# Kernel optimization log

Hardware: AMD Instinct MI355X
Metric: run time of the kernel (lower is better)

The kernel has to match this reference:

```python
import jax, jax.numpy as jnp
import numpy as np

# Involution2D config (matches init_kwargs)
F = 256          # filters
K = 3            # kernel_size
G = 16           # groups
RR = 4           # reduce_ratio
BN_EPS = 1e-3    # keras BatchNormalization default epsilon


def setup_inputs() -> dict:
    key = jax.random.key(0)
    ks = jax.random.split(key, 8)
    C = 256
    Cr = F // RR                    # reduce_mapping channels = 64
    KKG = K * K * G                 # span_mapping channels = 144
    s = lambda k, sh, fan: jax.random.normal(k, sh, jnp.float32) * (1.0 / np.sqrt(fan))
    return {
        "x": jax.random.normal(ks[0], (4, 128, 128, C), jnp.float32),
        # reduce_mapping: 1x1 conv + BN(inference) + relu
        "Wr": s(ks[1], (C, Cr), C),
        "br": jnp.zeros((Cr,), jnp.float32),
        "gamma": jnp.ones((Cr,), jnp.float32),
        "beta": jnp.zeros((Cr,), jnp.float32),
        "mean": jax.random.normal(ks[2], (Cr,), jnp.float32) * 0.1,
        "var": jax.random.uniform(ks[3], (Cr,), jnp.float32, 0.5, 1.5),
        # span_mapping: 1x1 conv -> K*K*G dynamic weights
        "Ws": s(ks[4], (Cr, KKG), Cr),
        "bs": jnp.zeros((KKG,), jnp.float32),
        # initial_mapping: 1x1 conv -> F (applied since F != K*K*G)
        "Wi": s(ks[5], (C, F), C),
        "bi": jnp.zeros((F,), jnp.float32),
    }


def reference(x, Wr, br, gamma, beta, mean, var, Ws, bs, Wi, bi):
    B, H, W, _ = x.shape
    KK = K * K
    # reduce_mapping: 1x1 conv + BN(inference) + relu
    r = jnp.einsum('bhwc,cd->bhwd', x, Wr) + br
    r = jax.nn.relu((r - mean) * jax.lax.rsqrt(var + BN_EPS) * gamma + beta)
    # span_mapping: per-pixel dynamic kernel weights [B,H,W,KK*G] -> [B,H,W,G,1,KK]
    w = jnp.einsum('bhwd,dk->bhwk', r, Ws) + bs
    w = w.reshape(B, H, W, G, KK)[:, :, :, :, None, :]
    # initial_mapping: 1x1 conv -> F channels
    xi = jnp.einsum('bhwc,cf->bhwf', x, Wi) + bi
    # tf.image.extract_patches (SAME, stride=1, rate=1): layout is
    # (kernel_pos major, channel minor), i.e. flat index = kpos*F + c
    pad = (K - 1) // 2
    xp = jnp.pad(xi, ((0, 0), (pad, pad), (pad, pad), (0, 0)))
    patches = jnp.stack(
        [xp[:, i:i + H, j:j + W, :] for i in range(K) for j in range(K)],
        axis=3)                                   # [B,H,W,KK,F]
    # faithful to the original K.reshape of the flat [KK*F] axis
    patches = patches.reshape(B, H, W, G, F // G, KK)
    out = jnp.sum(w * patches, axis=-1)           # [B,H,W,G,F//G]
    return out.reshape(B, H, W, F)
```

## Files before the change

### kernel.cpp

```cpp
#include <hip/hip_runtime.h>

#define BN_EPS 1e-3f

typedef __attribute__((ext_vector_type(8))) short bf16x8;
typedef __attribute__((ext_vector_type(4))) float f32x4;

__device__ inline unsigned short f2b(float f) {
    unsigned int u = __float_as_uint(f);
    unsigned int r = (u + 0x7fffu + ((u >> 16) & 1u)) >> 16;
    return (unsigned short)r;
}
__device__ inline float b2f(unsigned short h) {
    return __uint_as_float(((unsigned int)h) << 16);
}

__global__ void k_prep(const float* __restrict__ Wi, const float* __restrict__ Wr,
                       const float* __restrict__ Ws,
                       unsigned short* __restrict__ Bt, unsigned short* __restrict__ Wst) {
    int t = blockIdx.x * 256 + threadIdx.x;
    if (t < 320 * 256) {
        int n = t >> 8, k = t & 255;
        float v = (n < 256) ? Wi[k * 256 + n] : Wr[k * 64 + (n - 256)];
        Bt[t] = f2b(v);
    } else {
        int t2 = t - 320 * 256;
        if (t2 < 144 * 64) {
            int n = t2 >> 6, k = t2 & 63;
            Wst[t2] = f2b(Ws[k * 144 + n]);
        }
    }
}

#define XIP 264
#define RS_OFF (180 * XIP)
#define RSP 72
#define WL_OFF (RS_OFF + 180 * RSP)
#define SMN (WL_OFF + 128 * 144)

__global__ __launch_bounds__(512, 2) void k_fused(
    const float* __restrict__ x, const unsigned short* __restrict__ Bt,
    const unsigned short* __restrict__ Wst,
    const float* __restrict__ bi, const float* __restrict__ br,
    const float* __restrict__ gamma, const float* __restrict__ beta,
    const float* __restrict__ mean, const float* __restrict__ var,
    const float* __restrict__ bs, float* __restrict__ out)
{
    __shared__ __attribute__((aligned(16))) unsigned short sm[SMN];
    const int tid = threadIdx.x;
    const int bx = blockIdx.x;
    const int w0 = (bx & 7) * 16;
    const int h0 = ((bx >> 3) & 15) * 8;
    const int bb = bx >> 7;

    const int wv = tid >> 6;
    const int lane = tid & 63;
    const int col = lane & 15;
    const int quad = lane >> 4;

    const float bi_v0 = bi[(2 * wv) * 16 + col];
    const float bi_v1 = bi[(2 * wv + 1) * 16 + col];
    const int dcl = (wv & 3) * 16 + col;
    const float brd = br[dcl];
    const float md  = mean[dcl];
    const float sc  = gamma[dcl] * rsqrtf(var[dcl] + BN_EPS);
    const float btv = beta[dcl];

    bf16x8 bx0[8], bx1[8], brr[8];
    {
        const unsigned short* p0 = &Bt[((2 * wv) * 16 + col) * 256];
        const unsigned short* p1 = &Bt[((2 * wv + 1) * 16 + col) * 256];
#pragma unroll
        for (int kc = 0; kc < 8; ++kc) {
            bx0[kc] = *(const bf16x8*)&p0[kc * 32 + quad * 8];
            bx1[kc] = *(const bf16x8*)&p1[kc * 32 + quad * 8];
        }
        if (wv < 4) {
            const unsigned short* pr = &Bt[((16 + wv) * 16 + col) * 256];
#pragma unroll
            for (int kc = 0; kc < 8; ++kc)
                brr[kc] = *(const bf16x8*)&pr[kc * 32 + quad * 8];
        }
    }

    const int chq = (tid & 15) * 4;

    float4 vcur[4];
    int hp_cur;
    {
        hp_cur = (tid >> 4);
        int r = hp_cur / 18, cc = hp_cur - r * 18;
        int gh = h0 - 1 + r, gw = w0 - 1 + cc;
        bool ok = (hp_cur < 180) && ((unsigned)gh < 128u) && ((unsigned)gw < 128u);
        if (ok) {
            const float* src = x + (((long long)(bb * 128 + gh)) * 128 + gw) * 256 + chq;
#pragma unroll
            for (int j = 0; j < 4; ++j) vcur[j] = *(const float4*)&src[j * 64];
        } else {
#pragma unroll
            for (int j = 0; j < 4; ++j) vcur[j] = (float4){0.f, 0.f, 0.f, 0.f};
        }
        if (hp_cur < 180) {
#pragma unroll
            for (int j = 0; j < 4; ++j) {
                uint2 pk;
                pk.x = (unsigned)f2b(vcur[j].x) | ((unsigned)f2b(vcur[j].y) << 16);
                pk.y = (unsigned)f2b(vcur[j].z) | ((unsigned)f2b(vcur[j].w) << 16);
                *(uint2*)&sm[hp_cur * XIP + chq + j * 64] = pk;
            }
        }
    }
    __syncthreads();

    for (int c = 0; c < 6; ++c) {
        float4 vn[4];
        int hp_n = 192;
        if (c < 5) {
            hp_n = (c + 1) * 32 + (tid >> 4);
            int r = hp_n / 18, cc = hp_n - r * 18;
            int gh = h0 - 1 + r, gw = w0 - 1 + cc;
            bool ok = (hp_n < 180) && ((unsigned)gh < 128u) && ((unsigned)gw < 128u);
            if (ok) {
                const float* src = x + (((long long)(bb * 128 + gh)) * 128 + gw) * 256 + chq;
#pragma unroll
                for (int j = 0; j < 4; ++j) vn[j] = *(const float4*)&src[j * 64];
            } else {
#pragma unroll
                for (int j = 0; j < 4; ++j) vn[j] = (float4){0.f, 0.f, 0.f, 0.f};
            }
        }

        f32x4 a00 = {0.f,0.f,0.f,0.f}, a01 = a00, a10 = a00, a11 = a00;
        f32x4 ar0 = a00, ar1 = a00;
        {
            const int rowA0 = (c * 32 + col) * XIP;
            const int rowA1 = (c * 32 + 16 + col) * XIP;
#pragma unroll
            for (int kc = 0; kc < 8; ++kc) {
                const int kb = kc * 32 + quad * 8;
                bf16x8 a0 = *(const bf16x8*)&sm[rowA0 + kb];
                bf16x8 a1 = *(const bf16x8*)&sm[rowA1 + kb];
                a00 = __builtin_amdgcn_mfma_f32_16x16x32_bf16(a0, bx0[kc], a00, 0, 0, 0);
                a10 = __builtin_amdgcn_mfma_f32_16x16x32_bf16(a1, bx0[kc], a10, 0, 0, 0);
                a01 = __builtin_amdgcn_mfma_f32_16x16x32_bf16(a0, bx1[kc], a01, 0, 0, 0);
                a11 = __builtin_amdgcn_mfma_f32_16x16x32_bf16(a1, bx1[kc], a11, 0, 0, 0);
                if (wv < 4) {
                    ar0 = __builtin_amdgcn_mfma_f32_16x16x32_bf16(a0, brr[kc], ar0, 0, 0, 0);
                    ar1 = __builtin_amdgcn_mfma_f32_16x16x32_bf16(a1, brr[kc], ar1, 0, 0, 0);
                }
            }
        }
        __syncthreads();

        if (c < 5 && hp_n < 180) {
#pragma unroll
            for (int j = 0; j < 4; ++j) {
                uint2 pk;
                pk.x = (unsigned)f2b(vn[j].x) | ((unsigned)f2b(vn[j].y) << 16);
                pk.y = (unsigned)f2b(vn[j].z) | ((unsigned)f2b(vn[j].w) << 16);
                *(uint2*)&sm[hp_n * XIP + chq + j * 64] = pk;
            }
        }

        {
            const int n0 = (2 * wv) * 16 + col;
            const int n1 = (2 * wv + 1) * 16 + col;
            const int rb = c * 32 + quad * 4;
#pragma unroll
            for (int rg = 0; rg < 4; ++rg) {
                const int r0 = rb + rg, r1 = rb + 16 + rg;
                if (r0 < 180) {
                    sm[r0 * XIP + n0] = f2b(a00[rg] + bi_v0);
                    sm[r0 * XIP + n1] = f2b(a01[rg] + bi_v1);
                }
                if (r1 < 180) {
                    sm[r1 * XIP + n0] = f2b(a10[rg] + bi_v0);
                    sm[r1 * XIP + n1] = f2b(a11[rg] + bi_v1);
                }
            }
            if (wv < 4) {
#pragma unroll
                for (int rg = 0; rg < 4; ++rg) {
                    const int r0 = rb + rg, r1 = rb + 16 + rg;
                    if (r0 < 180) {
                        float v = (ar0[rg] + brd - md) * sc + btv;
                        sm[RS_OFF + r0 * RSP + dcl] = f2b(fmaxf(v, 0.f));
                    }
                    if (r1 < 180) {
                        float v = (ar1[rg] + brd - md) * sc + btv;
                        sm[RS_OFF + r1 * RSP + dcl] = f2b(fmaxf(v, 0.f));
                    }
                }
            }
        }
        __syncthreads();
    }

    {
        f32x4 wacc[9];
#pragma unroll
        for (int j = 0; j < 9; ++j) wacc[j] = (f32x4){0.f, 0.f, 0.f, 0.f};
        const int arow = (19 + wv * 18 + col) * RSP;
#pragma unroll
        for (int kc = 0; kc < 2; ++kc) {
            const int kb = kc * 32 + quad * 8;
            bf16x8 ra = *(const bf16x8*)&sm[RS_OFF + arow + kb];
#pragma unroll
            for (int j = 0; j < 9; ++j) {
                bf16x8 wb = *(const bf16x8*)&Wst[(j * 16 + col) * 64 + kb];
                wacc[j] = __builtin_amdgcn_mfma_f32_16x16x32_bf16(ra, wb, wacc[j], 0, 0, 0);
            }
        }
#pragma unroll
        for (int j = 0; j < 9; ++j) {
            const int n = j * 16 + col;
            const float bv = bs[n];
            const int prow = wv * 16 + quad * 4;
#pragma unroll
            for (int rg = 0; rg < 4; ++rg)
                sm[WL_OFF + (prow + rg) * 144 + n] = f2b(wacc[j][rg] + bv);
        }
    }
    __syncthreads();

    {
        const int g = tid & 15;
        const int pb = tid >> 4;

        const int idx0 = g * 144;
        const int kp0  = idx0 >> 8;
        const int c0   = idx0 & 255;
        int len1 = 256 - c0; if (len1 > 144) len1 = 144;
        const int kp1  = kp0 + 1;
        const int koff0 = (kp0 / 3) * 18 + (kp0 % 3);
        const int koff1 = (kp1 <= 8) ? ((kp1 / 3) * 18 + (kp1 % 3)) : 0;

#pragma unroll
        for (int jj = 0; jj < 4; ++jj) {
            const int p = pb + 32 * jj;
            const int phb = (p >> 4) * 18 + (p & 15);
            const int base0 = (phb + koff0) * XIP + c0;
            const int base1 = (phb + koff1) * XIP;

            float wf[9];
#pragma unroll
            for (int kk = 0; kk < 9; ++kk)
                wf[kk] = b2f(sm[WL_OFF + p * 144 + g * 9 + kk]);

            float res[16];
            {
                int4 xv[9];
#pragma unroll
                for (int i = 0; i < 9; ++i) {
                    const int e = i * 8;
                    const int addr = (e < len1) ? (base0 + e) : (base1 + (e - len1));
                    xv[i] = *(const int4*)&sm[addr];
                }
#pragma unroll
                for (int f2 = 0; f2 < 8; ++f2) {
                    float a = 0.f;
#pragma unroll
                    for (int kk = 0; kk < 9; ++kk) {
                        const int e = f2 * 9 + kk;
                        const int word = ((const int*)&xv[e >> 3])[(e >> 1) & 3];
                        const unsigned short u = (e & 1) ? (unsigned short)(((unsigned)word) >> 16)
                                                         : (unsigned short)(word & 0xffff);
                        a += wf[kk] * b2f(u);
                    }
                    res[f2] = a;
                }
            }
            {
                int4 xv[9];
#pragma unroll
                for (int i = 9; i < 18; ++i) {
                    const int e = i * 8;
                    const int addr = (e < len1) ? (base0 + e) : (base1 + (e - len1));
                    xv[i - 9] = *(const int4*)&sm[addr];
                }
#pragma unroll
                for (int f2 = 8; f2 < 16; ++f2) {
                    float a = 0.f;
#pragma unroll
                    for (int kk = 0; kk < 9; ++kk) {
                        const int e = f2 * 9 + kk;
                        const int i = (e >> 3) - 9;
                        const int word = ((const int*)&xv[i])[(e >> 1) & 3];
                        const unsigned short u = (e & 1) ? (unsigned short)(((unsigned)word) >> 16)
                                                         : (unsigned short)(word & 0xffff);
                        a += wf[kk] * b2f(u);
                    }
                    res[f2] = a;
                }
            }

            const long long orow =
                (((long long)(bb * 128 + h0 + (p >> 4))) * 128 + (w0 + (p & 15))) * 256 + g * 16;
#pragma unroll
            for (int q = 0; q < 4; ++q) {
                float4 o = {res[q * 4 + 0], res[q * 4 + 1], res[q * 4 + 2], res[q * 4 + 3]};
                *(float4*)&out[orow + q * 4] = o;
            }
        }
    }
}

extern "C" void kernel_launch(void* const* d_in, const int* in_sizes, int n_in,
                              void* d_out, int out_size, void* d_ws, size_t ws_size,
                              hipStream_t stream) {
    const float* x     = (const float*)d_in[0];
    const float* Wr    = (const float*)d_in[1];
    const float* br    = (const float*)d_in[2];
    const float* gamma = (const float*)d_in[3];
    const float* beta  = (const float*)d_in[4];
    const float* mean  = (const float*)d_in[5];
    const float* var   = (const float*)d_in[6];
    const float* Ws    = (const float*)d_in[7];
    const float* bs    = (const float*)d_in[8];
    const float* Wi    = (const float*)d_in[9];
    const float* bi    = (const float*)d_in[10];
    float* out = (float*)d_out;

    unsigned char* ws = (unsigned char*)d_ws;
    unsigned short* Bt  = (unsigned short*)(ws + 0);
    unsigned short* Wst = (unsigned short*)(ws + 163840);

    k_prep<<<dim3(356), dim3(256), 0, stream>>>(Wi, Wr, Ws, Bt, Wst);
    k_fused<<<dim3(512), dim3(512), 0, stream>>>(
        x, Bt, Wst, bi, br, gamma, beta, mean, var, bs, out);
}
```

Measured before the change: 174.8 us.

## Double block to 1024 threads, giving each wave one output tile per stage

Grows the fused block from 8 to 16 waves. Each wave now computes one 16-column tile of the initial-mapping GEMM instead of two, and the x staging loads are spread across twice as many threads. The span-mapping GEMM is split between two wave halves, with one column tile computed redundantly by both. The involution stage handles half as many pixels per thread. The aim is more waves per CU to hide latency, since LDS use already limits the CU to one block. The risk is that the stricter launch bounds force fewer registers per thread and cause spills.

```diff
diff --git a/kernel.cpp b/kernel.cpp
--- a/kernel.cpp
+++ b/kernel.cpp
@@ -37,7 +37,7 @@
 #define WL_OFF (RS_OFF + 180 * RSP)
 #define SMN (WL_OFF + 128 * 144)
 
-__global__ __launch_bounds__(512, 2) void k_fused(
+__global__ __launch_bounds__(1024, 4) void k_fused(
     const float* __restrict__ x, const unsigned short* __restrict__ Bt,
     const unsigned short* __restrict__ Wst,
     const float* __restrict__ bi, const float* __restrict__ br,
@@ -57,23 +57,19 @@
     const int col = lane & 15;
     const int quad = lane >> 4;
 
-    const float bi_v0 = bi[(2 * wv) * 16 + col];
-    const float bi_v1 = bi[(2 * wv + 1) * 16 + col];
+    const float bi_v = bi[wv * 16 + col];
     const int dcl = (wv & 3) * 16 + col;
     const float brd = br[dcl];
     const float md  = mean[dcl];
     const float sc  = gamma[dcl] * rsqrtf(var[dcl] + BN_EPS);
     const float btv = beta[dcl];
 
-    bf16x8 bx0[8], bx1[8], brr[8];
+    bf16x8 bxA[8], brr[8];
     {
-        const unsigned short* p0 = &Bt[((2 * wv) * 16 + col) * 256];
-        const unsigned short* p1 = &Bt[((2 * wv + 1) * 16 + col) * 256];
-#pragma unroll
-        for (int kc = 0; kc < 8; ++kc) {
-            bx0[kc] = *(const bf16x8*)&p0[kc * 32 + quad * 8];
-            bx1[kc] = *(const bf16x8*)&p1[kc * 32 + quad * 8];
-        }
+        const unsigned short* p0 = &Bt[(wv * 16 + col) * 256];
+#pragma unroll
+        for (int kc = 0; kc < 8; ++kc)
+            bxA[kc] = *(const bf16x8*)&p0[kc * 32 + quad * 8];
         if (wv < 4) {
             const unsigned short* pr = &Bt[((16 + wv) * 16 + col) * 256];
 #pragma unroll
@@ -82,67 +78,62 @@
         }
     }
 
-    const int chq = (tid & 15) * 4;
-
-    float4 vcur[4];
-    int hp_cur;
+    const int chq = (tid & 31) * 4;
+
     {
-        hp_cur = (tid >> 4);
-        int r = hp_cur / 18, cc = hp_cur - r * 18;
+        int hp = tid >> 5;
+        int r = hp / 18, cc = hp - r * 18;
         int gh = h0 - 1 + r, gw = w0 - 1 + cc;
-        bool ok = (hp_cur < 180) && ((unsigned)gh < 128u) && ((unsigned)gw < 128u);
+        bool ok = ((unsigned)gh < 128u) && ((unsigned)gw < 128u);
+        float4 v0, v1;
         if (ok) {
             const float* src = x + (((long long)(bb * 128 + gh)) * 128 + gw) * 256 + chq;
-#pragma unroll
-            for (int j = 0; j < 4; ++j) vcur[j] = *(const float4*)&src[j * 64];
+            v0 = *(const float4*)&src[0];
+            v1 = *(const float4*)&src[128];
         } else {
-#pragma unroll
-            for (int j = 0; j < 4; ++j) vcur[j] = (float4){0.f, 0.f, 0.f, 0.f};
-        }
-        if (hp_cur < 180) {
-#pragma unroll
-            for (int j = 0; j < 4; ++j) {
-                uint2 pk;
-                pk.x = (unsigned)f2b(vcur[j].x) | ((unsigned)f2b(vcur[j].y) << 16);
-                pk.y = (unsigned)f2b(vcur[j].z) | ((unsigned)f2b(vcur[j].w) << 16);
-                *(uint2*)&sm[hp_cur * XIP + chq + j * 64] = pk;
-            }
-        }
+            v0 = (float4){0.f, 0.f, 0.f, 0.f};
+            v1 = v0;
+        }
+        uint2 pk;
+        pk.x = (unsigned)f2b(v0.x) | ((unsigned)f2b(v0.y) << 16);
+        pk.y = (unsigned)f2b(v0.z) | ((unsigned)f2b(v0.w) << 16);
+        *(uint2*)&sm[hp * XIP + chq] = pk;
+        pk.x = (unsigned)f2b(v1.x) | ((unsigned)f2b(v1.y) << 16);
+        pk.y = (unsigned)f2b(v1.z) | ((unsigned)f2b(v1.w) << 16);
+        *(uint2*)&sm[hp * XIP + chq + 128] = pk;
     }
     __syncthreads();
 
     for (int c = 0; c < 6; ++c) {
-        float4 vn[4];
+        float4 vn0, vn1;
         int hp_n = 192;
         if (c < 5) {
-            hp_n = (c + 1) * 32 + (tid >> 4);
+            hp_n = (c + 1) * 32 + (tid >> 5);
             int r = hp_n / 18, cc = hp_n - r * 18;
             int gh = h0 - 1 + r, gw = w0 - 1 + cc;
             bool ok = (hp_n < 180) && ((unsigned)gh < 128u) && ((unsigned)gw < 128u);
             if (ok) {
                 const float* src = x + (((long long)(bb * 128 + gh)) * 128 + gw) * 256 + chq;
-#pragma unroll
-                for (int j = 0; j < 4; ++j) vn[j] = *(const float4*)&src[j * 64];
+                vn0 = *(const float4*)&src[0];
+                vn1 = *(const float4*)&src[128];
             } else {
-#pragma unroll
-                for (int j = 0; j < 4; ++j) vn[j] = (float4){0.f, 0.f, 0.f, 0.f};
-            }
-        }
-
-        f32x4 a00 = {0.f,0.f,0.f,0.f}, a01 = a00, a10 = a00, a11 = a00;
-        f32x4 ar0 = a00, ar1 = a00;
+                vn0 = (float4){0.f, 0.f, 0.f, 0.f};
+                vn1 = vn0;
+            }
+        }
+
+        f32x4 acc0 = {0.f, 0.f, 0.f, 0.f}, acc1 = acc0;
+        f32x4 ar0 = acc0, ar1 = acc0;
         {
             const int rowA0 = (c * 32 + col) * XIP;
-            const int rowA1 = (c * 32 + 16 + col) * XIP;
+            const int rowA1 = rowA0 + 16 * XIP;
 #pragma unroll
             for (int kc = 0; kc < 8; ++kc) {
                 const int kb = kc * 32 + quad * 8;
                 bf16x8 a0 = *(const bf16x8*)&sm[rowA0 + kb];
                 bf16x8 a1 = *(const bf16x8*)&sm[rowA1 + kb];
-                a00 = __builtin_amdgcn_mfma_f32_16x16x32_bf16(a0, bx0[kc], a00, 0, 0, 0);
-                a10 = __builtin_amdgcn_mfma_f32_16x16x32_bf16(a1, bx0[kc], a10, 0, 0, 0);
-                a01 = __builtin_amdgcn_mfma_f32_16x16x32_bf16(a0, bx1[kc], a01, 0, 0, 0);
-                a11 = __builtin_amdgcn_mfma_f32_16x16x32_bf16(a1, bx1[kc], a11, 0, 0, 0);
+                acc0 = __builtin_amdgcn_mfma_f32_16x16x32_bf16(a0, bxA[kc], acc0, 0, 0, 0);
+                acc1 = __builtin_amdgcn_mfma_f32_16x16x32_bf16(a1, bxA[kc], acc1, 0, 0, 0);
                 if (wv < 4) {
                     ar0 = __builtin_amdgcn_mfma_f32_16x16x32_bf16(a0, brr[kc], ar0, 0, 0, 0);
                     ar1 = __builtin_amdgcn_mfma_f32_16x16x32_bf16(a1, brr[kc], ar1, 0, 0, 0);
@@ -152,35 +143,28 @@
         __syncthreads();
 
         if (c < 5 && hp_n < 180) {
-#pragma unroll
-            for (int j = 0; j < 4; ++j) {
-                uint2 pk;
-                pk.x = (unsigned)f2b(vn[j].x) | ((unsigned)f2b(vn[j].y) << 16);
-                pk.y = (unsigned)f2b(vn[j].z) | ((unsigned)f2b(vn[j].w) << 16);
-                *(uint2*)&sm[hp_n * XIP + chq + j * 64] = pk;
-            }
+            uint2 pk;
+            pk.x = (unsigned)f2b(vn0.x) | ((unsigned)f2b(vn0.y) << 16);
+            pk.y = (unsigned)f2b(vn0.z) | ((unsigned)f2b(vn0.w) << 16);
+            *(uint2*)&sm[hp_n * XIP + chq] = pk;
+            pk.x = (unsigned)f2b(vn1.x) | ((unsigned)f2b(vn1.y) << 16);
+            pk.y = (unsigned)f2b(vn1.z) | ((unsigned)f2b(vn1.w) << 16);
+            *(uint2*)&sm[hp_n * XIP + chq + 128] = pk;
         }
 
         {
-            const int n0 = (2 * wv) * 16 + col;
-            const int n1 = (2 * wv + 1) * 16 + col;
+            const int n0 = wv * 16 + col;
             const int rb = c * 32 + quad * 4;
 #pragma unroll
             for (int rg = 0; rg < 4; ++rg) {
-                const int r0 = rb + rg, r1 = rb + 16 + rg;
-                if (r0 < 180) {
-                    sm[r0 * XIP + n0] = f2b(a00[rg] + bi_v0);
-                    sm[r0 * XIP + n1] = f2b(a01[rg] + bi_v1);
-                }
-                if (r1 < 180) {
-                    sm[r1 * XIP + n0] = f2b(a10[rg] + bi_v0);
-                    sm[r1 * XIP + n1] = f2b(a11[rg] + bi_v1);
-                }
+                const int r0 = rb + rg, r1 = r0 + 16;
+                if (r0 < 180) sm[r0 * XIP + n0] = f2b(acc0[rg] + bi_v);
+                if (r1 < 180) sm[r1 * XIP + n0] = f2b(acc1[rg] + bi_v);
             }
             if (wv < 4) {
 #pragma unroll
                 for (int rg = 0; rg < 4; ++rg) {
-                    const int r0 = rb + rg, r1 = rb + 16 + rg;
+                    const int r0 = rb + rg, r1 = r0 + 16;
                     if (r0 < 180) {
                         float v = (ar0[rg] + brd - md) * sc + btv;
                         sm[RS_OFF + r0 * RSP + dcl] = f2b(fmaxf(v, 0.f));
@@ -196,28 +180,30 @@
     }
 
     {
-        f32x4 wacc[9];
-#pragma unroll
-        for (int j = 0; j < 9; ++j) wacc[j] = (f32x4){0.f, 0.f, 0.f, 0.f};
-        const int arow = (19 + wv * 18 + col) * RSP;
+        const int m = wv & 7;
+        const int jbase = (wv >> 3) * 4;
+        f32x4 wacc[5];
+#pragma unroll
+        for (int jj = 0; jj < 5; ++jj) wacc[jj] = (f32x4){0.f, 0.f, 0.f, 0.f};
+        const int arow = (19 + m * 18 + col) * RSP;
 #pragma unroll
         for (int kc = 0; kc < 2; ++kc) {
             const int kb = kc * 32 + quad * 8;
             bf16x8 ra = *(const bf16x8*)&sm[RS_OFF + arow + kb];
 #pragma unroll
-            for (int j = 0; j < 9; ++j) {
-                bf16x8 wb = *(const bf16x8*)&Wst[(j * 16 + col) * 64 + kb];
-                wacc[j] = __builtin_amdgcn_mfma_f32_16x16x32_bf16(ra, wb, wacc[j], 0, 0, 0);
-            }
-        }
-#pragma unroll
-        for (int j = 0; j < 9; ++j) {
-            const int n = j * 16 + col;
+            for (int jj = 0; jj < 5; ++jj) {
+                bf16x8 wb = *(const bf16x8*)&Wst[((jbase + jj) * 16 + col) * 64 + kb];
+                wacc[jj] = __builtin_amdgcn_mfma_f32_16x16x32_bf16(ra, wb, wacc[jj], 0, 0, 0);
+            }
+        }
+#pragma unroll
+        for (int jj = 0; jj < 5; ++jj) {
+            const int n = (jbase + jj) * 16 + col;
             const float bv = bs[n];
-            const int prow = wv * 16 + quad * 4;
+            const int prow = m * 16 + quad * 4;
 #pragma unroll
             for (int rg = 0; rg < 4; ++rg)
-                sm[WL_OFF + (prow + rg) * 144 + n] = f2b(wacc[j][rg] + bv);
+                sm[WL_OFF + (prow + rg) * 144 + n] = f2b(wacc[jj][rg] + bv);
         }
     }
     __syncthreads();
@@ -235,8 +221,8 @@
         const int koff1 = (kp1 <= 8) ? ((kp1 / 3) * 18 + (kp1 % 3)) : 0;
 
 #pragma unroll
-        for (int jj = 0; jj < 4; ++jj) {
-            const int p = pb + 32 * jj;
+        for (int jj = 0; jj < 2; ++jj) {
+            const int p = pb + 64 * jj;
             const int phb = (p >> 4) * 18 + (p & 15);
             const int base0 = (phb + koff0) * XIP + c0;
             const int base1 = (phb + koff1) * XIP;
@@ -325,6 +311,6 @@
     unsigned short* Wst = (unsigned short*)(ws + 163840);
 
     k_prep<<<dim3(356), dim3(256), 0, stream>>>(Wi, Wr, Ws, Bt, Wst);
-    k_fused<<<dim3(512), dim3(512), 0, stream>>>(
+    k_fused<<<dim3(512), dim3(1024), 0, stream>>>(
         x, Bt, Wst, bi, br, gamma, beta, mean, var, bs, out);
 }
```

Result: slower. 179.1 us (+2.4%).

## Split fused involution kernel into GEMM pass and halo gather pass

Applied to the files above, without the earlier changes.

The single fused kernel, which recomputed the 1x1 projections over a halo of 180 pixels per 128-pixel tile, is split into two kernels. The first computes xi and the dynamic weights for 64 pixels per block without halo and writes them to the workspace as bf16. The second gathers an 8x8 tile plus halo from global memory and applies the involution. This removes redundant halo GEMM work and cuts shared memory so more blocks fit per CU, at the cost of a round trip through global memory of about 50 MB of intermediates and an extra launch.

```diff
diff --git a/kernel.cpp b/kernel.cpp
--- a/kernel.cpp
+++ b/kernel.cpp
@@ -31,193 +31,177 @@
     }
 }
 
-#define XIP 264
-#define RS_OFF (180 * XIP)
-#define RSP 72
-#define WL_OFF (RS_OFF + 180 * RSP)
-#define SMN (WL_OFF + 128 * 144)
-
-__global__ __launch_bounds__(512, 2) void k_fused(
+#define AXIP 264
+#define ARS_OFF (64 * AXIP)
+#define ASMN (ARS_OFF + 64 * 72)
+
+__global__ __launch_bounds__(256, 3) void k_xiw(
     const float* __restrict__ x, const unsigned short* __restrict__ Bt,
     const unsigned short* __restrict__ Wst,
     const float* __restrict__ bi, const float* __restrict__ br,
     const float* __restrict__ gamma, const float* __restrict__ beta,
     const float* __restrict__ mean, const float* __restrict__ var,
-    const float* __restrict__ bs, float* __restrict__ out)
+    const float* __restrict__ bs,
+    unsigned short* __restrict__ xi_g, unsigned short* __restrict__ w_g)
 {
-    __shared__ __attribute__((aligned(16))) unsigned short sm[SMN];
+    __shared__ __attribute__((aligned(16))) unsigned short sm[ASMN];
     const int tid = threadIdx.x;
-    const int bx = blockIdx.x;
-    const int w0 = (bx & 7) * 16;
-    const int h0 = ((bx >> 3) & 15) * 8;
-    const int bb = bx >> 7;
+    const long long px0 = (long long)blockIdx.x * 64;
 
     const int wv = tid >> 6;
     const int lane = tid & 63;
     const int col = lane & 15;
     const int quad = lane >> 4;
 
-    const float bi_v0 = bi[(2 * wv) * 16 + col];
-    const float bi_v1 = bi[(2 * wv + 1) * 16 + col];
-    const int dcl = (wv & 3) * 16 + col;
-    const float brd = br[dcl];
-    const float md  = mean[dcl];
-    const float sc  = gamma[dcl] * rsqrtf(var[dcl] + BN_EPS);
-    const float btv = beta[dcl];
-
-    bf16x8 bx0[8], bx1[8], brr[8];
-    {
-        const unsigned short* p0 = &Bt[((2 * wv) * 16 + col) * 256];
-        const unsigned short* p1 = &Bt[((2 * wv + 1) * 16 + col) * 256];
-#pragma unroll
-        for (int kc = 0; kc < 8; ++kc) {
-            bx0[kc] = *(const bf16x8*)&p0[kc * 32 + quad * 8];
-            bx1[kc] = *(const bf16x8*)&p1[kc * 32 + quad * 8];
-        }
-        if (wv < 4) {
-            const unsigned short* pr = &Bt[((16 + wv) * 16 + col) * 256];
-#pragma unroll
-            for (int kc = 0; kc < 8; ++kc)
-                brr[kc] = *(const bf16x8*)&pr[kc * 32 + quad * 8];
-        }
-    }
-
-    const int chq = (tid & 15) * 4;
-
-    float4 vcur[4];
-    int hp_cur;
-    {
-        hp_cur = (tid >> 4);
-        int r = hp_cur / 18, cc = hp_cur - r * 18;
-        int gh = h0 - 1 + r, gw = w0 - 1 + cc;
-        bool ok = (hp_cur < 180) && ((unsigned)gh < 128u) && ((unsigned)gw < 128u);
-        if (ok) {
-            const float* src = x + (((long long)(bb * 128 + gh)) * 128 + gw) * 256 + chq;
-#pragma unroll
-            for (int j = 0; j < 4; ++j) vcur[j] = *(const float4*)&src[j * 64];
+#pragma unroll
+    for (int it = 0; it < 8; ++it) {
+        const int flat = it * 256 + tid;
+        const int px = flat >> 5;
+        const int cho = (flat & 31) * 8;
+        const float* src = x + (px0 + px) * 256 + cho;
+        float4 v0 = *(const float4*)&src[0];
+        float4 v1 = *(const float4*)&src[4];
+        int4 pk;
+        pk.x = (int)((unsigned)f2b(v0.x) | ((unsigned)f2b(v0.y) << 16));
+        pk.y = (int)((unsigned)f2b(v0.z) | ((unsigned)f2b(v0.w) << 16));
+        pk.z = (int)((unsigned)f2b(v1.x) | ((unsigned)f2b(v1.y) << 16));
+        pk.w = (int)((unsigned)f2b(v1.z) | ((unsigned)f2b(v1.w) << 16));
+        *(int4*)&sm[px * AXIP + cho] = pk;
+    }
+    __syncthreads();
+
+    f32x4 acc[5][4];
+#pragma unroll
+    for (int jj = 0; jj < 5; ++jj)
+#pragma unroll
+        for (int m = 0; m < 4; ++m) acc[jj][m] = (f32x4){0.f, 0.f, 0.f, 0.f};
+
+#pragma unroll
+    for (int kc = 0; kc < 8; ++kc) {
+        const int kb = kc * 32 + quad * 8;
+        bf16x8 a[4];
+#pragma unroll
+        for (int m = 0; m < 4; ++m)
+            a[m] = *(const bf16x8*)&sm[(m * 16 + col) * AXIP + kb];
+#pragma unroll
+        for (int jj = 0; jj < 5; ++jj) {
+            const int j = wv * 5 + jj;
+            bf16x8 b = *(const bf16x8*)&Bt[(j * 16 + col) * 256 + kb];
+#pragma unroll
+            for (int m = 0; m < 4; ++m)
+                acc[jj][m] = __builtin_amdgcn_mfma_f32_16x16x32_bf16(a[m], b, acc[jj][m], 0, 0, 0);
+        }
+    }
+    __syncthreads();
+
+#pragma unroll
+    for (int jj = 0; jj < 5; ++jj) {
+        const int j = wv * 5 + jj;
+        if (j < 16) {
+            const int n = j * 16 + col;
+            const float bv = bi[n];
+#pragma unroll
+            for (int m = 0; m < 4; ++m)
+#pragma unroll
+                for (int rg = 0; rg < 4; ++rg) {
+                    const int row = m * 16 + quad * 4 + rg;
+                    sm[row * AXIP + n] = f2b(acc[jj][m][rg] + bv);
+                }
         } else {
-#pragma unroll
-            for (int j = 0; j < 4; ++j) vcur[j] = (float4){0.f, 0.f, 0.f, 0.f};
-        }
-        if (hp_cur < 180) {
-#pragma unroll
-            for (int j = 0; j < 4; ++j) {
-                uint2 pk;
-                pk.x = (unsigned)f2b(vcur[j].x) | ((unsigned)f2b(vcur[j].y) << 16);
-                pk.y = (unsigned)f2b(vcur[j].z) | ((unsigned)f2b(vcur[j].w) << 16);
-                *(uint2*)&sm[hp_cur * XIP + chq + j * 64] = pk;
+            const int d = (j - 16) * 16 + col;
+            const float sc = gamma[d] * rsqrtf(var[d] + BN_EPS);
+            const float bb2 = (br[d] - mean[d]) * sc + beta[d];
+#pragma unroll
+            for (int m = 0; m < 4; ++m)
+#pragma unroll
+                for (int rg = 0; rg < 4; ++rg) {
+                    const int row = m * 16 + quad * 4 + rg;
+                    const float v = acc[jj][m][rg] * sc + bb2;
+                    sm[ARS_OFF + row * 72 + d] = f2b(fmaxf(v, 0.f));
+                }
+        }
+    }
+    __syncthreads();
+
+    f32x4 wa[9];
+#pragma unroll
+    for (int j = 0; j < 9; ++j) wa[j] = (f32x4){0.f, 0.f, 0.f, 0.f};
+#pragma unroll
+    for (int kc = 0; kc < 2; ++kc) {
+        const int kb = kc * 32 + quad * 8;
+        bf16x8 ra = *(const bf16x8*)&sm[ARS_OFF + (wv * 16 + col) * 72 + kb];
+#pragma unroll
+        for (int j = 0; j < 9; ++j) {
+            bf16x8 wb = *(const bf16x8*)&Wst[(j * 16 + col) * 64 + kb];
+            wa[j] = __builtin_amdgcn_mfma_f32_16x16x32_bf16(ra, wb, wa[j], 0, 0, 0);
+        }
+    }
+
+#pragma unroll
+    for (int it = 0; it < 8; ++it) {
+        const int flat = it * 256 + tid;
+        const int px = flat >> 5;
+        const int cho = (flat & 31) * 8;
+        int4 v = *(const int4*)&sm[px * AXIP + cho];
+        *(int4*)&xi_g[(px0 + px) * 256 + cho] = v;
+    }
+
+#pragma unroll
+    for (int j = 0; j < 9; ++j) {
+        const int n = j * 16 + col;
+        const float bv = bs[n];
+#pragma unroll
+        for (int rg = 0; rg < 4; ++rg) {
+            const int row = wv * 16 + quad * 4 + rg;
+            w_g[(px0 + row) * 144 + n] = f2b(wa[j][rg] + bv);
+        }
+    }
+}
+
+#define GXIP 264
+#define GWL_OFF (100 * GXIP)
+#define GSMN (GWL_OFF + 64 * 144)
+
+__global__ __launch_bounds__(512, 4) void k_gather(
+    const unsigned short* __restrict__ xi_g, const unsigned short* __restrict__ w_g,
+    float* __restrict__ out)
+{
+    __shared__ __attribute__((aligned(16))) unsigned short sm[GSMN];
+    const int tid = threadIdx.x;
+    const int b = blockIdx.x;
+    const int bx = (b & 7) * 128 + (b >> 3);
+    const int w0 = (bx & 15) * 8;
+    const int h0 = ((bx >> 4) & 15) * 8;
+    const int bb = bx >> 8;
+
+#pragma unroll
+    for (int it = 0; it < 7; ++it) {
+        const int flat = it * 512 + tid;
+        if (flat < 3200) {
+            const int px = flat >> 5;
+            const int cho = (flat & 31) * 8;
+            const int hr = px / 10, hc = px - hr * 10;
+            const int gh = h0 - 1 + hr, gw = w0 - 1 + hc;
+            int4 v;
+            if (((unsigned)gh < 128u) && ((unsigned)gw < 128u)) {
+                const long long pxg = ((long long)(bb * 128 + gh)) * 128 + gw;
+                v = *(const int4*)&xi_g[pxg * 256 + cho];
+            } else {
+                v = (int4){0, 0, 0, 0};
             }
-        }
-    }
-    __syncthreads();
-
-    for (int c = 0; c < 6; ++c) {
-        float4 vn[4];
-        int hp_n = 192;
-        if (c < 5) {
-            hp_n = (c + 1) * 32 + (tid >> 4);
-            int r = hp_n / 18, cc = hp_n - r * 18;
-            int gh = h0 - 1 + r, gw = w0 - 1 + cc;
-            bool ok = (hp_n < 180) && ((unsigned)gh < 128u) && ((unsigned)gw < 128u);
-            if (ok) {
-                const float* src = x + (((long long)(bb * 128 + gh)) * 128 + gw) * 256 + chq;
-#pragma unroll
-                for (int j = 0; j < 4; ++j) vn[j] = *(const float4*)&src[j * 64];
-            } else {
-#pragma unroll
-                for (int j = 0; j < 4; ++j) vn[j] = (float4){0.f, 0.f, 0.f, 0.f};
-            }
-        }
-
-        f32x4 a00 = {0.f,0.f,0.f,0.f}, a01 = a00, a10 = a00, a11 = a00;
-        f32x4 ar0 = a00, ar1 = a00;
-        {
-            const int rowA0 = (c * 32 + col) * XIP;
-            const int rowA1 = (c * 32 + 16 + col) * XIP;
-#pragma unroll
-            for (int kc = 0; kc < 8; ++kc) {
-                const int kb = kc * 32 + quad * 8;
-                bf16x8 a0 = *(const bf16x8*)&sm[rowA0 + kb];
-                bf16x8 a1 = *(const bf16x8*)&sm[rowA1 + kb];
-                a00 = __builtin_amdgcn_mfma_f32_16x16x32_bf16(a0, bx0[kc], a00, 0, 0, 0);
-                a10 = __builtin_amdgcn_mfma_f32_16x16x32_bf16(a1, bx0[kc], a10, 0, 0, 0);
-                a01 = __builtin_amdgcn_mfma_f32_16x16x32_bf16(a0, bx1[kc], a01, 0, 0, 0);
-                a11 = __builtin_amdgcn_mfma_f32_16x16x32_bf16(a1, bx1[kc], a11, 0, 0, 0);
-                if (wv < 4) {
-                    ar0 = __builtin_amdgcn_mfma_f32_16x16x32_bf16(a0, brr[kc], ar0, 0, 0, 0);
-                    ar1 = __builtin_amdgcn_mfma_f32_16x16x32_bf16(a1, brr[kc], ar1, 0, 0, 0);
-                }
-            }
-        }
-        __syncthreads();
-
-        if (c < 5 && hp_n < 180) {
-#pragma unroll
-            for (int j = 0; j < 4; ++j) {
-                uint2 pk;
-                pk.x = (unsigned)f2b(vn[j].x) | ((unsigned)f2b(vn[j].y) << 16);
-                pk.y = (unsigned)f2b(vn[j].z) | ((unsigned)f2b(vn[j].w) << 16);
-                *(uint2*)&sm[hp_n * XIP + chq + j * 64] = pk;
-            }
-        }
-
-        {
-            const int n0 = (2 * wv) * 16 + col;
-            const int n1 = (2 * wv + 1) * 16 + col;
-            const int rb = c * 32 + quad * 4;
-#pragma unroll
-            for (int rg = 0; rg < 4; ++rg) {
-                const int r0 = rb + rg, r1 = rb + 16 + rg;
-                if (r0 < 180) {
-                    sm[r0 * XIP + n0] = f2b(a00[rg] + bi_v0);
-                    sm[r0 * XIP + n1] = f2b(a01[rg] + bi_v1);
-                }
-                if (r1 < 180) {
-                    sm[r1 * XIP + n0] = f2b(a10[rg] + bi_v0);
-                    sm[r1 * XIP + n1] = f2b(a11[rg] + bi_v1);
-                }
-            }
-            if (wv < 4) {
-#pragma unroll
-                for (int rg = 0; rg < 4; ++rg) {
-                    const int r0 = rb + rg, r1 = rb + 16 + rg;
-                    if (r0 < 180) {
-                        float v = (ar0[rg] + brd - md) * sc + btv;
-                        sm[RS_OFF + r0 * RSP + dcl] = f2b(fmaxf(v, 0.f));
-                    }
-                    if (r1 < 180) {
-                        float v = (ar1[rg] + brd - md) * sc + btv;
-                        sm[RS_OFF + r1 * RSP + dcl] = f2b(fmaxf(v, 0.f));
-                    }
-                }
-            }
-        }
-        __syncthreads();
-    }
-
-    {
-        f32x4 wacc[9];
-#pragma unroll
-        for (int j = 0; j < 9; ++j) wacc[j] = (f32x4){0.f, 0.f, 0.f, 0.f};
-        const int arow = (19 + wv * 18 + col) * RSP;
-#pragma unroll
-        for (int kc = 0; kc < 2; ++kc) {
-            const int kb = kc * 32 + quad * 8;
-            bf16x8 ra = *(const bf16x8*)&sm[RS_OFF + arow + kb];
-#pragma unroll
-            for (int j = 0; j < 9; ++j) {
-                bf16x8 wb = *(const bf16x8*)&Wst[(j * 16 + col) * 64 + kb];
-                wacc[j] = __builtin_amdgcn_mfma_f32_16x16x32_bf16(ra, wb, wacc[j], 0, 0, 0);
-            }
-        }
-#pragma unroll
-        for (int j = 0; j < 9; ++j) {
-            const int n = j * 16 + col;
-            const float bv = bs[n];
-            const int prow = wv * 16 + quad * 4;
-#pragma unroll
-            for (int rg = 0; rg < 4; ++rg)
-                sm[WL_OFF + (prow + rg) * 144 + n] = f2b(wacc[j][rg] + bv);
+            *(int4*)&sm[px * GXIP + cho] = v;
+        }
+    }
+#pragma unroll
+    for (int it = 0; it < 3; ++it) {
+        const int flat = it * 512 + tid;
+        if (flat < 1152) {
+            const int px = flat / 18;
+            const int cho = (flat - px * 18) * 8;
+            const long long pxg =
+                ((long long)(bb * 128 + h0 + (px >> 3))) * 128 + (w0 + (px & 7));
+            int4 v = *(const int4*)&w_g[pxg * 144 + cho];
+            *(int4*)&sm[GWL_OFF + px * 144 + cho] = v;
         }
     }
     __syncthreads();
@@ -231,20 +215,20 @@
         const int c0   = idx0 & 255;
         int len1 = 256 - c0; if (len1 > 144) len1 = 144;
         const int kp1  = kp0 + 1;
-        const int koff0 = (kp0 / 3) * 18 + (kp0 % 3);
-        const int koff1 = (kp1 <= 8) ? ((kp1 / 3) * 18 + (kp1 % 3)) : 0;
-
-#pragma unroll
-        for (int jj = 0; jj < 4; ++jj) {
+        const int koff0 = (kp0 / 3) * 10 + (kp0 % 3);
+        const int koff1 = (kp1 <= 8) ? ((kp1 / 3) * 10 + (kp1 % 3)) : 0;
+
+#pragma unroll
+        for (int jj = 0; jj < 2; ++jj) {
             const int p = pb + 32 * jj;
-            const int phb = (p >> 4) * 18 + (p & 15);
-            const int base0 = (phb + koff0) * XIP + c0;
-            const int base1 = (phb + koff1) * XIP;
+            const int phb = (p >> 3) * 10 + (p & 7);
+            const int base0 = (phb + koff0) * GXIP + c0;
+            const int base1 = (phb + koff1) * GXIP;
 
             float wf[9];
 #pragma unroll
             for (int kk = 0; kk < 9; ++kk)
-                wf[kk] = b2f(sm[WL_OFF + p * 144 + g * 9 + kk]);
+                wf[kk] = b2f(sm[GWL_OFF + p * 144 + g * 9 + kk]);
 
             float res[16];
             {
@@ -294,7 +278,7 @@
             }
 
             const long long orow =
-                (((long long)(bb * 128 + h0 + (p >> 4))) * 128 + (w0 + (p & 15))) * 256 + g * 16;
+                (((long long)(bb * 128 + h0 + (p >> 3))) * 128 + (w0 + (p & 7))) * 256 + g * 16;
 #pragma unroll
             for (int q = 0; q < 4; ++q) {
                 float4 o = {res[q * 4 + 0], res[q * 4 + 1], res[q * 4 + 2], res[q * 4 + 3]};
@@ -321,10 +305,13 @@
     float* out = (float*)d_out;
 
     unsigned char* ws = (unsigned char*)d_ws;
-    unsigned short* Bt  = (unsigned short*)(ws + 0);
-    unsigned short* Wst = (unsigned short*)(ws + 163840);
+    unsigned short* Bt   = (unsigned short*)(ws + 0);
+    unsigned short* Wst  = (unsigned short*)(ws + 163840);
+    unsigned short* xi_g = (unsigned short*)(ws + 182272);
+    unsigned short* w_g  = (unsigned short*)(ws + 33736704);
 
     k_prep<<<dim3(356), dim3(256), 0, stream>>>(Wi, Wr, Ws, Bt, Wst);
-    k_fused<<<dim3(512), dim3(512), 0, stream>>>(
-        x, Bt, Wst, bi, br, gamma, beta, mean, var, bs, out);
-}
+    k_xiw<<<dim3(1024), dim3(256), 0, stream>>>(
+        x, Bt, Wst, bi, br, gamma, beta, mean, var, bs, xi_g, w_g);
+    k_gather<<<dim3(1024), dim3(512), 0, stream>>>(xi_g, w_g, out);
+}
```

After: 196.3 us. +12.3%, slower.
